# Kernel tuning notes

Measured on AMD Instinct MI355X. Metric: run time of the kernel, lower is better.

Reference implementation:

```python
import jax, jax.numpy as jnp
import numpy as np

INPUT_DIM, DIM, N_ACTIONS = 2048, 1024, 64
B, T = 1024, 16

def setup_inputs() -> dict:
    key = jax.random.key(0)
    ks = jax.random.split(key, 8)
    s = 1.0 / np.sqrt(INPUT_DIM)
    return {
        "precondition": jax.random.normal(ks[0], (B, T, INPUT_DIM), jnp.float32),
        "effect": jax.random.normal(ks[1], (B, T, INPUT_DIM), jnp.float32),
        "action": jax.random.randint(ks[2], (B,), 0, N_ACTIONS, jnp.int32),
        "Wp": jax.random.uniform(ks[3], (DIM, INPUT_DIM), jnp.float32, -s, s),
        "bp": jax.random.uniform(ks[4], (DIM,), jnp.float32, -s, s),
        "We": jax.random.uniform(ks[5], (DIM, INPUT_DIM), jnp.float32, -s, s),
        "be": jax.random.uniform(ks[6], (DIM,), jnp.float32, -s, s),
        "W_trans": jax.random.normal(ks[7], (N_ACTIONS, DIM, DIM), jnp.float32) * 0.02,
    }

def reference(precondition, effect, action, Wp, bp, We, be, W_trans):
    # mean-pool over time
    p_avg = precondition.mean(axis=1)  # [B, input_dim]
    e_avg = effect.mean(axis=1)        # [B, input_dim]
    # linear projections
    p_embed = p_avg @ Wp.T + bp        # [B, dim]
    e_embed = e_avg @ We.T + be        # [B, dim]
    # gather per-sample transformation matrix, then batched matvec
    sel = W_trans[action]              # [B, dim, dim]
    p_t = jnp.einsum('bij,bj->bi', sel, p_embed)  # [B, dim]
    # torch: bmm(...).unsqueeze(1) on [B, dim, 1] -> [B, 1, dim, 1]
    p_transformed = p_t[:, None, :, None]
    return (p_transformed, e_embed)
```

## Files before the change

### kernel.cpp

```cpp
#include <hip/hip_runtime.h>
#include <stdint.h>

#define IDIM 2048
#define ODIM 1024
#define NACT 64
#define NB 1024
#define NT 16

typedef __attribute__((ext_vector_type(8))) short short8;
typedef __attribute__((ext_vector_type(4))) float floatx4;

__device__ __forceinline__ unsigned short f2bf(float f) {
    union { float f; unsigned u; } v; v.f = f;
    unsigned r = v.u + 0x7FFFu + ((v.u >> 16) & 1u);
    return (unsigned short)(r >> 16);
}

__global__ __launch_bounds__(256) void k_avg(const float* __restrict__ p,
                                             const float* __restrict__ e,
                                             unsigned short* __restrict__ pavg,
                                             unsigned short* __restrict__ eavg) {
    int idx = blockIdx.x * 256 + threadIdx.x;
    int b  = idx >> 9;
    int d4 = idx & 511;
    const float4* pr = (const float4*)(p + (size_t)b * (NT * IDIM)) + d4;
    const float4* er = (const float4*)(e + (size_t)b * (NT * IDIM)) + d4;
    float sx=0, sy=0, sz=0, sw=0, tx=0, ty=0, tz=0, tw=0;
#pragma unroll
    for (int t = 0; t < NT; ++t) {
        float4 a = pr[t * (IDIM/4)];
        float4 c = er[t * (IDIM/4)];
        sx += a.x; sy += a.y; sz += a.z; sw += a.w;
        tx += c.x; ty += c.y; tz += c.z; tw += c.w;
    }
    const float s = 1.0f / NT;
    ushort4 op = make_ushort4(f2bf(sx*s), f2bf(sy*s), f2bf(sz*s), f2bf(sw*s));
    ushort4 oe = make_ushort4(f2bf(tx*s), f2bf(ty*s), f2bf(tz*s), f2bf(tw*s));
    *(ushort4*)(pavg + (size_t)b*IDIM + d4*4) = op;
    *(ushort4*)(eavg + (size_t)b*IDIM + d4*4) = oe;
}

__global__ __launch_bounds__(256) void k_cvt(const float* __restrict__ w,
                                             unsigned short* __restrict__ o) {
    int idx = blockIdx.x * 256 + threadIdx.x;
    float4 v = ((const float4*)w)[idx];
    *(ushort4*)(o + (size_t)idx*4) = make_ushort4(f2bf(v.x), f2bf(v.y), f2bf(v.z), f2bf(v.w));
}

__global__ void k_group(const int* __restrict__ action,
                        int* __restrict__ order, int* __restrict__ starts) {
    __shared__ int cnt[NACT], cnt2[NACT], base[NACT];
    int t = threadIdx.x;
    if (t < NACT) { cnt[t] = 0; cnt2[t] = 0; }
    __syncthreads();
    int a = action[t];
    atomicAdd(&cnt[a], 1);
    __syncthreads();
    if (t < NACT) {
        int s = 0;
        for (int j = 0; j < t; ++j) s += cnt[j];
        base[t] = s;
        starts[t] = s;
        if (t == NACT - 1) starts[NACT] = s + cnt[t];
    }
    __syncthreads();
    int pos = base[a] + atomicAdd(&cnt2[a], 1);
    order[pos] = t;
}

__global__ __launch_bounds__(256) void k_embed(const unsigned short* __restrict__ pavg,
                                               const unsigned short* __restrict__ eavg,
                                               const unsigned short* __restrict__ wpb,
                                               const unsigned short* __restrict__ web,
                                               const float* __restrict__ bp,
                                               const float* __restrict__ be,
                                               unsigned short* __restrict__ peb,
                                               float* __restrict__ eout) {
    const int z = blockIdx.z;
    const unsigned short* Ag = z ? eavg : pavg;
    const unsigned short* Wg = z ? web  : wpb;
    const float* bias        = z ? be   : bp;
    const int row0 = blockIdx.x * 128;
    const int col0 = blockIdx.y * 64;
    __shared__ unsigned short As[128*40];
    __shared__ unsigned short Bs[64*40];
    const int tid  = threadIdx.x;
    const int w    = tid >> 6, lane = tid & 63;
    const int lr   = lane & 15, quad = lane >> 4;
    floatx4 acc[2][4];
#pragma unroll
    for (int s = 0; s < 2; ++s)
#pragma unroll
        for (int t = 0; t < 4; ++t) { floatx4 zz = {0.f,0.f,0.f,0.f}; acc[s][t] = zz; }

    const int rA0 = tid >> 2,        pA0 = tid & 3;
    const int rA1 = (tid+256) >> 2,  pA1 = tid & 3;

    for (int ks = 0; ks < IDIM/32; ++ks) {
        const int k0 = ks * 32;
        int4 a0 = *(const int4*)(Ag + (size_t)(row0 + rA0)*IDIM + k0 + pA0*8);
        int4 a1 = *(const int4*)(Ag + (size_t)(row0 + rA1)*IDIM + k0 + pA1*8);
        int4 b0 = *(const int4*)(Wg + (size_t)(col0 + rA0)*IDIM + k0 + pA0*8);
        __syncthreads();
        *(int4*)(&As[rA0*40 + pA0*8]) = a0;
        *(int4*)(&As[rA1*40 + pA1*8]) = a1;
        *(int4*)(&Bs[rA0*40 + pA0*8]) = b0;
        __syncthreads();
        short8 af[2], bf[4];
#pragma unroll
        for (int s = 0; s < 2; ++s)
            af[s] = *(const short8*)&As[(w*32 + s*16 + lr)*40 + quad*8];
#pragma unroll
        for (int t = 0; t < 4; ++t)
            bf[t] = *(const short8*)&Bs[(t*16 + lr)*40 + quad*8];
#pragma unroll
        for (int s = 0; s < 2; ++s)
#pragma unroll
            for (int t = 0; t < 4; ++t)
                acc[s][t] = __builtin_amdgcn_mfma_f32_16x16x32_bf16(af[s], bf[t], acc[s][t], 0, 0, 0);
    }

#pragma unroll
    for (int s = 0; s < 2; ++s) {
        const int rg = row0 + w*32 + s*16 + quad*4;
#pragma unroll
        for (int t = 0; t < 4; ++t) {
            const int cg = col0 + t*16 + lr;
            const float bv = bias[cg];
#pragma unroll
            for (int r = 0; r < 4; ++r) {
                float val = acc[s][t][r] + bv;
                if (z) eout[(size_t)(rg + r)*ODIM + cg] = val;
                else   peb[(size_t)(rg + r)*ODIM + cg] = f2bf(val);
            }
        }
    }
}

__global__ __launch_bounds__(256) void k_trans(const float* __restrict__ Wt,
                                               const unsigned short* __restrict__ peb,
                                               const int* __restrict__ order,
                                               const int* __restrict__ starts,
                                               float* __restrict__ out) {
    const int a  = blockIdx.z;
    const int g0 = starts[a], g1 = starts[a+1];
    const int gs = g0 + blockIdx.y * 32;
    int nb = g1 - gs;
    if (nb <= 0) return;
    if (nb > 32) nb = 32;
    const int i0 = blockIdx.x * 128;
    const float* M = Wt + (size_t)a * ODIM * ODIM;
    __shared__ unsigned short Ms[128*40];
    __shared__ unsigned short Ps[32*40];
    __shared__ int sorder[32];
    const int tid = threadIdx.x;
    if (tid < 32) sorder[tid] = order[gs + (tid < nb ? tid : 0)];
    __syncthreads();
    const int w  = tid >> 6, lane = tid & 63;
    const int lr = lane & 15, quad = lane >> 4;
    const int prw = sorder[(tid >> 2) & 31];
    floatx4 acc[2][2];
#pragma unroll
    for (int s = 0; s < 2; ++s)
#pragma unroll
        for (int t = 0; t < 2; ++t) { floatx4 zz = {0.f,0.f,0.f,0.f}; acc[s][t] = zz; }

    for (int ks = 0; ks < ODIM/32; ++ks) {
        const int k0 = ks * 32;
        float4 mv[4];
#pragma unroll
        for (int u = 0; u < 4; ++u) {
            int c = tid + u*256;
            int r = c >> 3, pt = c & 7;
            mv[u] = *(const float4*)(M + (size_t)(i0 + r)*ODIM + k0 + pt*4);
        }
        int4 pv;
        if (tid < 128) {
            int pt = tid & 3;
            pv = *(const int4*)(peb + (size_t)prw*ODIM + k0 + pt*8);
        }
        __syncthreads();
#pragma unroll
        for (int u = 0; u < 4; ++u) {
            int c = tid + u*256;
            int r = c >> 3, pt = c & 7;
            *(ushort4*)(&Ms[r*40 + pt*4]) =
                make_ushort4(f2bf(mv[u].x), f2bf(mv[u].y), f2bf(mv[u].z), f2bf(mv[u].w));
        }
        if (tid < 128) {
            int r = tid >> 2, pt = tid & 3;
            *(int4*)(&Ps[r*40 + pt*8]) = pv;
        }
        __syncthreads();
        short8 af[2], bf[2];
#pragma unroll
        for (int s = 0; s < 2; ++s)
            af[s] = *(const short8*)&Ms[(w*32 + s*16 + lr)*40 + quad*8];
#pragma unroll
        for (int t = 0; t < 2; ++t)
            bf[t] = *(const short8*)&Ps[(t*16 + lr)*40 + quad*8];
#pragma unroll
        for (int s = 0; s < 2; ++s)
#pragma unroll
            for (int t = 0; t < 2; ++t)
                acc[s][t] = __builtin_amdgcn_mfma_f32_16x16x32_bf16(af[s], bf[t], acc[s][t], 0, 0, 0);
    }

#pragma unroll
    for (int t = 0; t < 2; ++t) {
        int bb = t*16 + lr;
        if (bb < nb) {
            int bg = sorder[bb];
#pragma unroll
            for (int s = 0; s < 2; ++s) {
                int ig = i0 + w*32 + s*16 + quad*4;
                float4 v = make_float4(acc[s][t][0], acc[s][t][1], acc[s][t][2], acc[s][t][3]);
                *(float4*)(out + (size_t)bg*ODIM + ig) = v;
            }
        }
    }
}

extern "C" void kernel_launch(void* const* d_in, const int* in_sizes, int n_in,
                              void* d_out, int out_size, void* d_ws, size_t ws_size,
                              hipStream_t stream) {
    const float* prec = (const float*)d_in[0];
    const float* eff  = (const float*)d_in[1];
    const int*   act  = (const int*)d_in[2];
    const float* Wp   = (const float*)d_in[3];
    const float* bp   = (const float*)d_in[4];
    const float* We   = (const float*)d_in[5];
    const float* be   = (const float*)d_in[6];
    const float* Wt   = (const float*)d_in[7];
    float* out = (float*)d_out;

    uint8_t* ws = (uint8_t*)d_ws;
    unsigned short* pavg = (unsigned short*)(ws + 0);
    unsigned short* eavg = (unsigned short*)(ws + 4194304);
    unsigned short* wpb  = (unsigned short*)(ws + 8388608);
    unsigned short* web  = (unsigned short*)(ws + 12582912);
    unsigned short* peb  = (unsigned short*)(ws + 16777216);
    int* order  = (int*)(ws + 18874368);
    int* starts = order + NB;

    hipLaunchKernelGGL(k_avg,   dim3(2048),     dim3(256),  0, stream, prec, eff, pavg, eavg);
    hipLaunchKernelGGL(k_cvt,   dim3(2048),     dim3(256),  0, stream, Wp, wpb);
    hipLaunchKernelGGL(k_cvt,   dim3(2048),     dim3(256),  0, stream, We, web);
    hipLaunchKernelGGL(k_group, dim3(1),        dim3(1024), 0, stream, act, order, starts);
    hipLaunchKernelGGL(k_embed, dim3(8,16,2),   dim3(256),  0, stream,
                       pavg, eavg, wpb, web, bp, be, peb, out + 1048576);
    hipLaunchKernelGGL(k_trans, dim3(8,32,64),  dim3(256),  0, stream,
                       Wt, peb, order, starts, out);
}
```

Measured before the change: 621.3 us.

## Load MFMA fragments directly from global, merge weight conversion, shrink transform grid

The embedding and per-action transform kernels no longer stage tiles through shared memory. Each lane now loads its MFMA operand fragments straight from global memory, with the loop unrolled by two, which removes both __syncthreads barriers per k-step. The two weight-conversion launches become one kernel covering both matrices. The transform grid's group dimension drops from 32 to 4, so far fewer empty blocks are launched. In exchange, each action group can now hold at most 128 samples, and operands shared across waves are re-fetched from global or cache instead of reused from LDS.

```diff
diff --git a/kernel.cpp b/kernel.cpp
--- a/kernel.cpp
+++ b/kernel.cpp
@@ -14,6 +14,15 @@
     union { float f; unsigned u; } v; v.f = f;
     unsigned r = v.u + 0x7FFFu + ((v.u >> 16) & 1u);
     return (unsigned short)(r >> 16);
+}
+
+__device__ __forceinline__ short8 pack_bf8(float4 a, float4 b) {
+    short8 r;
+    r[0] = (short)f2bf(a.x); r[1] = (short)f2bf(a.y);
+    r[2] = (short)f2bf(a.z); r[3] = (short)f2bf(a.w);
+    r[4] = (short)f2bf(b.x); r[5] = (short)f2bf(b.y);
+    r[6] = (short)f2bf(b.z); r[7] = (short)f2bf(b.w);
+    return r;
 }
 
 __global__ __launch_bounds__(256) void k_avg(const float* __restrict__ p,
@@ -40,11 +49,16 @@
     *(ushort4*)(eavg + (size_t)b*IDIM + d4*4) = oe;
 }
 
-__global__ __launch_bounds__(256) void k_cvt(const float* __restrict__ w,
-                                             unsigned short* __restrict__ o) {
+__global__ __launch_bounds__(256) void k_cvt(const float* __restrict__ wp,
+                                             const float* __restrict__ we,
+                                             unsigned short* __restrict__ op,
+                                             unsigned short* __restrict__ oe) {
     int idx = blockIdx.x * 256 + threadIdx.x;
-    float4 v = ((const float4*)w)[idx];
-    *(ushort4*)(o + (size_t)idx*4) = make_ushort4(f2bf(v.x), f2bf(v.y), f2bf(v.z), f2bf(v.w));
+    const float4* src; unsigned short* dst; int j;
+    if (idx < (ODIM*IDIM/4)) { src = (const float4*)wp; dst = op; j = idx; }
+    else                     { src = (const float4*)we; dst = oe; j = idx - (ODIM*IDIM/4); }
+    float4 v = src[j];
+    *(ushort4*)(dst + (size_t)j*4) = make_ushort4(f2bf(v.x), f2bf(v.y), f2bf(v.z), f2bf(v.w));
 }
 
 __global__ void k_group(const int* __restrict__ action,
@@ -82,42 +96,34 @@
     const float* bias        = z ? be   : bp;
     const int row0 = blockIdx.x * 128;
     const int col0 = blockIdx.y * 64;
-    __shared__ unsigned short As[128*40];
-    __shared__ unsigned short Bs[64*40];
     const int tid  = threadIdx.x;
     const int w    = tid >> 6, lane = tid & 63;
     const int lr   = lane & 15, quad = lane >> 4;
+
+    const unsigned short* a0p = Ag + (size_t)(row0 + w*32 + lr) * IDIM + quad*8;
+    const unsigned short* a1p = a0p + (size_t)16 * IDIM;
+    const unsigned short* bq  = Wg + quad*8;
+
     floatx4 acc[2][4];
 #pragma unroll
     for (int s = 0; s < 2; ++s)
 #pragma unroll
         for (int t = 0; t < 4; ++t) { floatx4 zz = {0.f,0.f,0.f,0.f}; acc[s][t] = zz; }
 
-    const int rA0 = tid >> 2,        pA0 = tid & 3;
-    const int rA1 = (tid+256) >> 2,  pA1 = tid & 3;
-
+#pragma unroll 2
     for (int ks = 0; ks < IDIM/32; ++ks) {
         const int k0 = ks * 32;
-        int4 a0 = *(const int4*)(Ag + (size_t)(row0 + rA0)*IDIM + k0 + pA0*8);
-        int4 a1 = *(const int4*)(Ag + (size_t)(row0 + rA1)*IDIM + k0 + pA1*8);
-        int4 b0 = *(const int4*)(Wg + (size_t)(col0 + rA0)*IDIM + k0 + pA0*8);
-        __syncthreads();
-        *(int4*)(&As[rA0*40 + pA0*8]) = a0;
-        *(int4*)(&As[rA1*40 + pA1*8]) = a1;
-        *(int4*)(&Bs[rA0*40 + pA0*8]) = b0;
-        __syncthreads();
-        short8 af[2], bf[4];
-#pragma unroll
-        for (int s = 0; s < 2; ++s)
-            af[s] = *(const short8*)&As[(w*32 + s*16 + lr)*40 + quad*8];
+        short8 af0 = *(const short8*)(a0p + k0);
+        short8 af1 = *(const short8*)(a1p + k0);
+        short8 bf[4];
 #pragma unroll
         for (int t = 0; t < 4; ++t)
-            bf[t] = *(const short8*)&Bs[(t*16 + lr)*40 + quad*8];
-#pragma unroll
-        for (int s = 0; s < 2; ++s)
-#pragma unroll
-            for (int t = 0; t < 4; ++t)
-                acc[s][t] = __builtin_amdgcn_mfma_f32_16x16x32_bf16(af[s], bf[t], acc[s][t], 0, 0, 0);
+            bf[t] = *(const short8*)(bq + (size_t)(col0 + t*16 + lr)*IDIM + k0);
+#pragma unroll
+        for (int t = 0; t < 4; ++t) {
+            acc[0][t] = __builtin_amdgcn_mfma_f32_16x16x32_bf16(af0, bf[t], acc[0][t], 0, 0, 0);
+            acc[1][t] = __builtin_amdgcn_mfma_f32_16x16x32_bf16(af1, bf[t], acc[1][t], 0, 0, 0);
+        }
     }
 
 #pragma unroll
@@ -149,68 +155,48 @@
     if (nb <= 0) return;
     if (nb > 32) nb = 32;
     const int i0 = blockIdx.x * 128;
-    const float* M = Wt + (size_t)a * ODIM * ODIM;
-    __shared__ unsigned short Ms[128*40];
-    __shared__ unsigned short Ps[32*40];
-    __shared__ int sorder[32];
     const int tid = threadIdx.x;
-    if (tid < 32) sorder[tid] = order[gs + (tid < nb ? tid : 0)];
-    __syncthreads();
     const int w  = tid >> 6, lane = tid & 63;
     const int lr = lane & 15, quad = lane >> 4;
-    const int prw = sorder[(tid >> 2) & 31];
+
+    const float* M  = Wt + (size_t)a * ODIM * ODIM;
+    const float* m0 = M + (size_t)(i0 + w*32 + lr) * ODIM + quad*8;
+    const float* m1 = m0 + (size_t)16 * ODIM;
+
+    const int c0 = lr, c1 = 16 + lr;
+    const int b0 = order[gs + (c0 < nb ? c0 : 0)];
+    const int b1 = order[gs + (c1 < nb ? c1 : 0)];
+    const unsigned short* p0 = peb + (size_t)b0 * ODIM + quad*8;
+    const unsigned short* p1 = peb + (size_t)b1 * ODIM + quad*8;
+
     floatx4 acc[2][2];
 #pragma unroll
     for (int s = 0; s < 2; ++s)
 #pragma unroll
         for (int t = 0; t < 2; ++t) { floatx4 zz = {0.f,0.f,0.f,0.f}; acc[s][t] = zz; }
 
+#pragma unroll 2
     for (int ks = 0; ks < ODIM/32; ++ks) {
         const int k0 = ks * 32;
-        float4 mv[4];
-#pragma unroll
-        for (int u = 0; u < 4; ++u) {
-            int c = tid + u*256;
-            int r = c >> 3, pt = c & 7;
-            mv[u] = *(const float4*)(M + (size_t)(i0 + r)*ODIM + k0 + pt*4);
-        }
-        int4 pv;
-        if (tid < 128) {
-            int pt = tid & 3;
-            pv = *(const int4*)(peb + (size_t)prw*ODIM + k0 + pt*8);
-        }
-        __syncthreads();
-#pragma unroll
-        for (int u = 0; u < 4; ++u) {
-            int c = tid + u*256;
-            int r = c >> 3, pt = c & 7;
-            *(ushort4*)(&Ms[r*40 + pt*4]) =
-                make_ushort4(f2bf(mv[u].x), f2bf(mv[u].y), f2bf(mv[u].z), f2bf(mv[u].w));
-        }
-        if (tid < 128) {
-            int r = tid >> 2, pt = tid & 3;
-            *(int4*)(&Ps[r*40 + pt*8]) = pv;
-        }
-        __syncthreads();
-        short8 af[2], bf[2];
-#pragma unroll
-        for (int s = 0; s < 2; ++s)
-            af[s] = *(const short8*)&Ms[(w*32 + s*16 + lr)*40 + quad*8];
-#pragma unroll
-        for (int t = 0; t < 2; ++t)
-            bf[t] = *(const short8*)&Ps[(t*16 + lr)*40 + quad*8];
-#pragma unroll
-        for (int s = 0; s < 2; ++s)
-#pragma unroll
-            for (int t = 0; t < 2; ++t)
-                acc[s][t] = __builtin_amdgcn_mfma_f32_16x16x32_bf16(af[s], bf[t], acc[s][t], 0, 0, 0);
+        float4 xa = *(const float4*)(m0 + k0);
+        float4 xb = *(const float4*)(m0 + k0 + 4);
+        float4 ya = *(const float4*)(m1 + k0);
+        float4 yb = *(const float4*)(m1 + k0 + 4);
+        short8 pf0 = *(const short8*)(p0 + k0);
+        short8 pf1 = *(const short8*)(p1 + k0);
+        short8 af0 = pack_bf8(xa, xb);
+        short8 af1 = pack_bf8(ya, yb);
+        acc[0][0] = __builtin_amdgcn_mfma_f32_16x16x32_bf16(af0, pf0, acc[0][0], 0, 0, 0);
+        acc[0][1] = __builtin_amdgcn_mfma_f32_16x16x32_bf16(af0, pf1, acc[0][1], 0, 0, 0);
+        acc[1][0] = __builtin_amdgcn_mfma_f32_16x16x32_bf16(af1, pf0, acc[1][0], 0, 0, 0);
+        acc[1][1] = __builtin_amdgcn_mfma_f32_16x16x32_bf16(af1, pf1, acc[1][1], 0, 0, 0);
     }
 
 #pragma unroll
     for (int t = 0; t < 2; ++t) {
         int bb = t*16 + lr;
         if (bb < nb) {
-            int bg = sorder[bb];
+            int bg = t ? b1 : b0;
 #pragma unroll
             for (int s = 0; s < 2; ++s) {
                 int ig = i0 + w*32 + s*16 + quad*4;
@@ -244,11 +230,10 @@
     int* starts = order + NB;
 
     hipLaunchKernelGGL(k_avg,   dim3(2048),     dim3(256),  0, stream, prec, eff, pavg, eavg);
-    hipLaunchKernelGGL(k_cvt,   dim3(2048),     dim3(256),  0, stream, Wp, wpb);
-    hipLaunchKernelGGL(k_cvt,   dim3(2048),     dim3(256),  0, stream, We, web);
+    hipLaunchKernelGGL(k_cvt,   dim3(4096),     dim3(256),  0, stream, Wp, We, wpb, web);
     hipLaunchKernelGGL(k_group, dim3(1),        dim3(1024), 0, stream, act, order, starts);
     hipLaunchKernelGGL(k_embed, dim3(8,16,2),   dim3(256),  0, stream,
                        pavg, eavg, wpb, web, bp, be, peb, out + 1048576);
-    hipLaunchKernelGGL(k_trans, dim3(8,32,64),  dim3(256),  0, stream,
+    hipLaunchKernelGGL(k_trans, dim3(8,4,64),   dim3(256),  0, stream,
                        Wt, peb, order, starts, out);
 }
```

Result: slower. 684.3 us (+10.1%).
